# Kernel optimization log

Hardware: AMD Instinct MI355X
Metric: run time of the kernel (lower is better)

## Reference

```python
import jax, jax.numpy as jnp
import numpy as np

B, T, D, E, H = 4, 1024, 1024, 8, 2048


def setup_inputs() -> dict:
    key = jax.random.key(0)
    ks = jax.random.split(key, 5)
    # Kaiming-uniform-ish init scales (exact values irrelevant for correctness baseline)
    bound_bank = 1.0 / np.sqrt(D)
    bound_down = 1.0 / np.sqrt(H)
    return {
        "x": jax.random.normal(ks[0], (B, T, D), dtype=jnp.float32),
        "gate_w": jax.random.uniform(ks[1], (E, D), jnp.float32, -bound_bank, bound_bank),
        "gate_bank": jax.random.uniform(ks[2], (E, D, H), jnp.float32, -bound_bank, bound_bank),
        "up_bank": jax.random.uniform(ks[3], (E, D, H), jnp.float32, -bound_bank, bound_bank),
        "down_bank": jax.random.uniform(ks[4], (E, H, D), jnp.float32, -bound_down, bound_down),
    }


def reference(x, gate_w, gate_bank, up_bank, down_bank):
    # Router logits: [B,T,E] (nn.Linear with weight [E,D], no bias)
    logits = jnp.einsum('btd,ed->bte', x, gate_w)
    selected = jnp.argmax(logits, axis=-1)          # [B,T] int
    # Dense all-expert SwiGLU
    u = jnp.einsum('btd,edh->bteh', x, up_bank)     # [B,T,E,H]
    a = jnp.einsum('btd,edh->bteh', x, gate_bank)   # [B,T,E,H]
    h = jax.nn.silu(a) * u                          # [B,T,E,H]
    y = jnp.einsum('bteh,ehd->bted', h, down_bank)  # [B,T,E,D]
    # Gather argmax-selected expert output per token
    idx = selected[:, :, None, None]                # [B,T,1,1]
    out = jnp.take_along_axis(y, idx, axis=2)[:, :, 0, :]  # [B,T,D]
    return out
```

## Files before the change

kernel.cpp:

```cpp
#include <hip/hip_runtime.h>
#include <hip/hip_bf16.h>

#define NTOK 4096
#define DDIM 1024
#define HDIM 2048
#define NEXP 8

typedef __attribute__((ext_vector_type(4))) float f32x4;
typedef __attribute__((ext_vector_type(8))) short bf16x8;
typedef __attribute__((ext_vector_type(8))) unsigned short us8;

__device__ __forceinline__ unsigned short f2bf(float f) {
    unsigned u = __float_as_uint(f);
    return (unsigned short)((u + 0x7fffu + ((u >> 16) & 1u)) >> 16);
}

__device__ __forceinline__ void gload16(const void* g, void* l) {
    __builtin_amdgcn_global_load_lds((const __attribute__((address_space(1))) void*)g,
                                     (__attribute__((address_space(3))) void*)l, 16, 0, 0);
}

__global__ __launch_bounds__(256) void xg_kernel(
        const float* __restrict__ x, const float* __restrict__ gw,
        unsigned short* __restrict__ xb, int* __restrict__ sel) {
    const int t = blockIdx.x, tid = threadIdx.x, lane = tid & 63, w = tid >> 6;
    const float4 v = *reinterpret_cast<const float4*>(x + (size_t)t * DDIM + tid * 4);
    ushort4 o = { f2bf(v.x), f2bf(v.y), f2bf(v.z), f2bf(v.w) };
    *reinterpret_cast<ushort4*>(xb + (size_t)t * DDIM + tid * 4) = o;

    double acc[NEXP];
    #pragma unroll
    for (int e = 0; e < NEXP; ++e) {
        const float4 g = *reinterpret_cast<const float4*>(gw + (size_t)e * DDIM + tid * 4);
        acc[e] = (double)v.x * g.x + (double)v.y * g.y + (double)v.z * g.z + (double)v.w * g.w;
    }
    __shared__ double red[4][NEXP];
    #pragma unroll
    for (int e = 0; e < NEXP; ++e) {
        double a = acc[e];
        #pragma unroll
        for (int off = 32; off; off >>= 1) a += __shfl_down(a, off);
        if (lane == 0) red[w][e] = a;
    }
    __syncthreads();
    if (tid == 0) {
        int best = 0; double bv = -1e300;
        #pragma unroll
        for (int e = 0; e < NEXP; ++e) {
            double s = red[0][e] + red[1][e] + red[2][e] + red[3][e];
            if (s > bv) { bv = s; best = e; }
        }
        sel[t] = best;
    }
}

__global__ void scatter_kernel(const int* __restrict__ sel, int* __restrict__ cnt,
                               int* __restrict__ perm) {
    int t = blockIdx.x * blockDim.x + threadIdx.x;
    if (t < NTOK) {
        int e = sel[t];
        int p = atomicAdd(&cnt[e], 1);
        perm[e * NTOK + p] = t;
    }
}

__global__ __launch_bounds__(256) void fcast(const float* __restrict__ src,
        unsigned short* __restrict__ dst, int R, int C, int NB, int KS,
        int interleave, int qsel, long long estride) {
    __shared__ unsigned short tile[64][72];
    const int e = blockIdx.z, r0 = blockIdx.y * 64, c0 = blockIdx.x * 64;
    const float* s = src + ((size_t)e * R + r0) * C + c0;
    const int t = threadIdx.x;
    const int rd = t >> 2;
    #pragma unroll
    for (int j = 0; j < 4; ++j) {
        int c4 = (t & 3) * 4 + j;
        float4 v = *reinterpret_cast<const float4*>(s + (size_t)rd * C + c4 * 4);
        tile[c4 * 4 + 0][rd] = f2bf(v.x);
        tile[c4 * 4 + 1][rd] = f2bf(v.y);
        tile[c4 * 4 + 2][rd] = f2bf(v.z);
        tile[c4 * 4 + 3][rd] = f2bf(v.w);
    }
    __syncthreads();
    const int q = t >> 6, l = t & 63, li = l & 15, lg = l >> 4;
    const int nblk = interleave ? (((c0 >> 4) + q) * 2 + qsel) : ((c0 >> 4) + q);
    #pragma unroll
    for (int kf2 = 0; kf2 < 2; ++kf2) {
        const int ks = (r0 >> 5) + kf2;
        us8 v = *reinterpret_cast<const us8*>(&tile[q * 16 + li][kf2 * 32 + lg * 8]);
        *reinterpret_cast<us8*>(dst + ((size_t)e * estride) +
            (((size_t)nblk * KS + ks) << 9) + l * 8) = v;
    }
}

__global__ __launch_bounds__(256, 3) void stage_a(
        const unsigned short* __restrict__ xb, const unsigned short* __restrict__ wa,
        const int* __restrict__ cnt, const int* __restrict__ perm,
        unsigned short* __restrict__ hws) {
    const int e = blockIdx.z;
    const int bx = blockIdx.x;
    const int m0 = blockIdx.y * 128;
    const int count = cnt[e];
    if (m0 >= count) return;
    const int* pl = perm + e * NTOK;

    __shared__ unsigned short __attribute__((aligned(16))) As[2][128 * 64];

    const int tid = threadIdx.x, lane = tid & 63, w = tid >> 6;
    const int wr = w >> 1, wc = w & 1, li = lane & 15, lg = lane >> 4;
    const int sb = lane & 7, r8 = lane >> 3;
    const int srcswz = (sb ^ r8) * 8;

    const unsigned short* pA[4];
    #pragma unroll
    for (int i = 0; i < 4; ++i) {
        int row = i * 32 + w * 8 + r8;
        int tr = m0 + row; if (tr >= count) tr = count - 1;
        pA[i] = xb + (size_t)pl[tr] * DDIM + srcswz;
    }
    const unsigned short* bp = wa + (((size_t)e * 256 + bx * 8 + wc * 4) << 5 << 9)
                               + (size_t)lane * 8;

    f32x4 acc[4][4];
    #pragma unroll
    for (int i = 0; i < 4; ++i)
        #pragma unroll
        for (int j = 0; j < 4; ++j) acc[i][j] = (f32x4){0.f, 0.f, 0.f, 0.f};

    #pragma unroll
    for (int i = 0; i < 4; ++i) gload16(pA[i], &As[0][(i * 256 + w * 64) * 8]);
    asm volatile("s_waitcnt vmcnt(0)" ::: "memory");
    __syncthreads();

    int cur = 0;
    const int NT = DDIM / 64;
    for (int t = 0; t < NT; ++t) {
        if (t + 1 < NT) {
            const int k0 = (t + 1) * 64;
            #pragma unroll
            for (int i = 0; i < 4; ++i) gload16(pA[i] + k0, &As[cur ^ 1][(i * 256 + w * 64) * 8]);
        }
        #pragma unroll
        for (int kf = 0; kf < 2; ++kf) {
            const int kb = kf * 4 + lg;
            bf16x8 a[4], b[4];
            #pragma unroll
            for (int ni = 0; ni < 4; ++ni)
                b[ni] = *reinterpret_cast<const bf16x8*>(bp + (((size_t)(ni * 32 + t * 2 + kf)) << 9));
            #pragma unroll
            for (int mi = 0; mi < 4; ++mi) {
                int r = wr * 64 + mi * 16 + li;
                a[mi] = *reinterpret_cast<const bf16x8*>(&As[cur][r * 64 + ((kb ^ (li & 7)) << 3)]);
            }
            #pragma unroll
            for (int mi = 0; mi < 4; ++mi)
                #pragma unroll
                for (int ni = 0; ni < 4; ++ni)
                    acc[mi][ni] = __builtin_amdgcn_mfma_f32_16x16x32_bf16(a[mi], b[ni], acc[mi][ni], 0, 0, 0);
        }
        if (t + 1 < NT) {
            asm volatile("s_waitcnt vmcnt(0)" ::: "memory");
            __syncthreads();
            cur ^= 1;
        }
    }
    const int hbase = bx * 64 + wc * 32 + li;
    #pragma unroll
    for (int mi = 0; mi < 4; ++mi) {
        #pragma unroll
        for (int r = 0; r < 4; ++r) {
            int row = m0 + wr * 64 + mi * 16 + lg * 4 + r;
            if (row < count) {
                int tok = pl[row];
                #pragma unroll
                for (int p = 0; p < 2; ++p) {
                    float a = acc[mi][p * 2 + 0][r];
                    float u = acc[mi][p * 2 + 1][r];
                    float h = (a / (1.f + __expf(-a))) * u;
                    hws[(size_t)tok * HDIM + hbase + p * 16] = f2bf(h);
                }
            }
        }
    }
}

__global__ __launch_bounds__(256, 3) void stage_b(
        const unsigned short* __restrict__ hws, const unsigned short* __restrict__ wb,
        const int* __restrict__ cnt, const int* __restrict__ perm,
        float* __restrict__ out) {
    const int e = blockIdx.z;
    const int bx = blockIdx.x;
    const int m0 = blockIdx.y * 128;
    const int count = cnt[e];
    if (m0 >= count) return;
    const int* pl = perm + e * NTOK;

    __shared__ unsigned short __attribute__((aligned(16))) As[2][128 * 64];

    const int tid = threadIdx.x, lane = tid & 63, w = tid >> 6;
    const int wr = w >> 1, wc = w & 1, li = lane & 15, lg = lane >> 4;
    const int sb = lane & 7, r8 = lane >> 3;
    const int srcswz = (sb ^ r8) * 8;

    const unsigned short* pA[4];
    #pragma unroll
    for (int i = 0; i < 4; ++i) {
        int row = i * 32 + w * 8 + r8;
        int tr = m0 + row; if (tr >= count) tr = count - 1;
        pA[i] = hws + (size_t)pl[tr] * HDIM + srcswz;
    }
    const unsigned short* bp = wb + (((size_t)e * 64 + bx * 8 + wc * 4) * 64 << 9)
                               + (size_t)lane * 8;

    f32x4 acc[4][4];
    #pragma unroll
    for (int i = 0; i < 4; ++i)
        #pragma unroll
        for (int j = 0; j < 4; ++j) acc[i][j] = (f32x4){0.f, 0.f, 0.f, 0.f};

    #pragma unroll
    for (int i = 0; i < 4; ++i) gload16(pA[i], &As[0][(i * 256 + w * 64) * 8]);
    asm volatile("s_waitcnt vmcnt(0)" ::: "memory");
    __syncthreads();

    int cur = 0;
    const int NT = HDIM / 64;
    for (int t = 0; t < NT; ++t) {
        if (t + 1 < NT) {
            const int k0 = (t + 1) * 64;
            #pragma unroll
            for (int i = 0; i < 4; ++i) gload16(pA[i] + k0, &As[cur ^ 1][(i * 256 + w * 64) * 8]);
        }
        #pragma unroll
        for (int kf = 0; kf < 2; ++kf) {
            const int kb = kf * 4 + lg;
            bf16x8 a[4], b[4];
            #pragma unroll
            for (int ni = 0; ni < 4; ++ni)
                b[ni] = *reinterpret_cast<const bf16x8*>(bp + (((size_t)(ni * 64 + t * 2 + kf)) << 9));
            #pragma unroll
            for (int mi = 0; mi < 4; ++mi) {
                int r = wr * 64 + mi * 16 + li;
                a[mi] = *reinterpret_cast<const bf16x8*>(&As[cur][r * 64 + ((kb ^ (li & 7)) << 3)]);
            }
            #pragma unroll
            for (int mi = 0; mi < 4; ++mi)
                #pragma unroll
                for (int ni = 0; ni < 4; ++ni)
                    acc[mi][ni] = __builtin_amdgcn_mfma_f32_16x16x32_bf16(a[mi], b[ni], acc[mi][ni], 0, 0, 0);
        }
        if (t + 1 < NT) {
            asm volatile("s_waitcnt vmcnt(0)" ::: "memory");
            __syncthreads();
            cur ^= 1;
        }
    }
    const int cbase = bx * 128 + wc * 64 + li;
    #pragma unroll
    for (int mi = 0; mi < 4; ++mi) {
        #pragma unroll
        for (int r = 0; r < 4; ++r) {
            int row = m0 + wr * 64 + mi * 16 + lg * 4 + r;
            if (row < count) {
                int tok = pl[row];
                #pragma unroll
                for (int ni = 0; ni < 4; ++ni)
                    out[(size_t)tok * DDIM + cbase + ni * 16] = acc[mi][ni][r];
            }
        }
    }
}

extern "C" void kernel_launch(void* const* d_in, const int* in_sizes, int n_in,
                              void* d_out, int out_size, void* d_ws, size_t ws_size,
                              hipStream_t stream) {
    const float* x  = (const float*)d_in[0];
    const float* gw = (const float*)d_in[1];
    const float* gb = (const float*)d_in[2];
    const float* ub = (const float*)d_in[3];
    const float* db = (const float*)d_in[4];
    float* out = (float*)d_out;

    char* ws = (char*)d_ws;
    unsigned short* wbank = (unsigned short*)(ws);
    unsigned short* hws   = (unsigned short*)(ws + 67108864);
    unsigned short* xbf   = (unsigned short*)(ws + 67108864 + 16777216);
    char* misc = ws + 67108864 + 16777216 + 8388608;
    int* cnt  = (int*)(misc);
    int* sel  = (int*)(misc + 256);
    int* perm = (int*)(misc + 256 + 16384);

    hipMemsetAsync(cnt, 0, 256, stream);
    xg_kernel<<<NTOK, 256, 0, stream>>>(x, gw, xbf, sel);
    fcast<<<dim3(HDIM / 64, DDIM / 64, NEXP), 256, 0, stream>>>(
        gb, wbank, DDIM, HDIM, 256, 32, 1, 0, (long long)256 * 32 * 512);
    fcast<<<dim3(HDIM / 64, DDIM / 64, NEXP), 256, 0, stream>>>(
        ub, wbank, DDIM, HDIM, 256, 32, 1, 1, (long long)256 * 32 * 512);
    scatter_kernel<<<NTOK / 256, 256, 0, stream>>>(sel, cnt, perm);
    stage_a<<<dim3(2 * HDIM / 128, NTOK / 128, NEXP), 256, 0, stream>>>(
        xbf, wbank, cnt, perm, hws);
    fcast<<<dim3(DDIM / 64, HDIM / 64, NEXP), 256, 0, stream>>>(
        db, wbank, HDIM, DDIM, 64, 64, 0, 0, (long long)64 * 64 * 512);
    stage_b<<<dim3(DDIM / 128, NTOK / 128, NEXP), 256, 0, stream>>>(
        hws, wbank, cnt, perm, out);
}
```

Before: 382.4 us.

## Split-K down projection with atomics, smaller tiles, and LDS-free weight cast

The down-projection kernel now uses 64-row tiles and splits the H reduction into two halves across grid z, so it launches more blocks to fill the device. Partial sums are combined with float atomicAdd into an output that is zeroed beforehand. The weight cast kernel drops its LDS transpose and reads strided columns directly into the packed bf16 layout, and both GEMM stages request occupancy 4. In exchange, the output is written twice through atomics and needs an extra memset, results become order-nondeterministic, and the cast's column reads are less coalesced.

```diff
diff --git a/kernel.cpp b/kernel.cpp
--- a/kernel.cpp
+++ b/kernel.cpp
@@ -65,35 +65,22 @@
 }
 
 __global__ __launch_bounds__(256) void fcast(const float* __restrict__ src,
-        unsigned short* __restrict__ dst, int R, int C, int NB, int KS,
+        unsigned short* __restrict__ dst, int C, int KS, int NB,
         int interleave, int qsel, long long estride) {
-    __shared__ unsigned short tile[64][72];
-    const int e = blockIdx.z, r0 = blockIdx.y * 64, c0 = blockIdx.x * 64;
-    const float* s = src + ((size_t)e * R + r0) * C + c0;
-    const int t = threadIdx.x;
-    const int rd = t >> 2;
-    #pragma unroll
-    for (int j = 0; j < 4; ++j) {
-        int c4 = (t & 3) * 4 + j;
-        float4 v = *reinterpret_cast<const float4*>(s + (size_t)rd * C + c4 * 4);
-        tile[c4 * 4 + 0][rd] = f2bf(v.x);
-        tile[c4 * 4 + 1][rd] = f2bf(v.y);
-        tile[c4 * 4 + 2][rd] = f2bf(v.z);
-        tile[c4 * 4 + 3][rd] = f2bf(v.w);
-    }
-    __syncthreads();
-    const int q = t >> 6, l = t & 63, li = l & 15, lg = l >> 4;
-    const int nblk = interleave ? (((c0 >> 4) + q) * 2 + qsel) : ((c0 >> 4) + q);
-    #pragma unroll
-    for (int kf2 = 0; kf2 < 2; ++kf2) {
-        const int ks = (r0 >> 5) + kf2;
-        us8 v = *reinterpret_cast<const us8*>(&tile[q * 16 + li][kf2 * 32 + lg * 8]);
-        *reinterpret_cast<us8*>(dst + ((size_t)e * estride) +
-            (((size_t)nblk * KS + ks) << 9) + l * 8) = v;
-    }
-}
-
-__global__ __launch_bounds__(256, 3) void stage_a(
+    const int e = blockIdx.z, cblk = blockIdx.x;
+    const int w = threadIdx.x >> 6, l = threadIdx.x & 63;
+    const int ks = blockIdx.y * 4 + w;
+    const int li = l & 15, lg = l >> 4;
+    const int nblk = interleave ? cblk * 2 + qsel : cblk;
+    const float* s = src + ((size_t)e * KS * 32 + ks * 32 + lg * 8) * C + cblk * 16 + li;
+    unsigned short v[8];
+    #pragma unroll
+    for (int j = 0; j < 8; ++j) v[j] = f2bf(s[(size_t)j * C]);
+    *reinterpret_cast<us8*>(dst + (size_t)e * estride +
+        (((size_t)nblk * KS + ks) << 9) + l * 8) = *reinterpret_cast<const us8*>(v);
+}
+
+__global__ __launch_bounds__(256, 4) void stage_a(
         const unsigned short* __restrict__ xb, const unsigned short* __restrict__ wa,
         const int* __restrict__ cnt, const int* __restrict__ perm,
         unsigned short* __restrict__ hws) {
@@ -184,69 +171,69 @@
     }
 }
 
-__global__ __launch_bounds__(256, 3) void stage_b(
+__global__ __launch_bounds__(256, 4) void stage_b(
         const unsigned short* __restrict__ hws, const unsigned short* __restrict__ wb,
         const int* __restrict__ cnt, const int* __restrict__ perm,
         float* __restrict__ out) {
-    const int e = blockIdx.z;
+    const int z = blockIdx.z, e = z >> 1, kz = z & 1;
     const int bx = blockIdx.x;
-    const int m0 = blockIdx.y * 128;
+    const int m0 = blockIdx.y * 64;
     const int count = cnt[e];
     if (m0 >= count) return;
     const int* pl = perm + e * NTOK;
 
-    __shared__ unsigned short __attribute__((aligned(16))) As[2][128 * 64];
-
-    const int tid = threadIdx.x, lane = tid & 63, w = tid >> 6;
-    const int wr = w >> 1, wc = w & 1, li = lane & 15, lg = lane >> 4;
+    __shared__ unsigned short __attribute__((aligned(16))) As[2][64 * 64];
+
+    const int tid = threadIdx.x, lane = tid & 63, wc = tid >> 6;
+    const int li = lane & 15, lg = lane >> 4;
     const int sb = lane & 7, r8 = lane >> 3;
     const int srcswz = (sb ^ r8) * 8;
 
-    const unsigned short* pA[4];
-    #pragma unroll
-    for (int i = 0; i < 4; ++i) {
-        int row = i * 32 + w * 8 + r8;
+    const unsigned short* pA[2];
+    #pragma unroll
+    for (int i = 0; i < 2; ++i) {
+        int row = wc * 16 + i * 8 + r8;
         int tr = m0 + row; if (tr >= count) tr = count - 1;
-        pA[i] = hws + (size_t)pl[tr] * HDIM + srcswz;
-    }
-    const unsigned short* bp = wb + (((size_t)e * 64 + bx * 8 + wc * 4) * 64 << 9)
-                               + (size_t)lane * 8;
-
-    f32x4 acc[4][4];
+        pA[i] = hws + (size_t)pl[tr] * HDIM + kz * 1024 + srcswz;
+    }
+    const unsigned short* bp = wb + ((((size_t)e * 64 + bx * 8 + wc * 2) * 64
+                               + (size_t)kz * 32) << 9) + (size_t)lane * 8;
+
+    f32x4 acc[4][2];
     #pragma unroll
     for (int i = 0; i < 4; ++i)
         #pragma unroll
-        for (int j = 0; j < 4; ++j) acc[i][j] = (f32x4){0.f, 0.f, 0.f, 0.f};
-
-    #pragma unroll
-    for (int i = 0; i < 4; ++i) gload16(pA[i], &As[0][(i * 256 + w * 64) * 8]);
+        for (int j = 0; j < 2; ++j) acc[i][j] = (f32x4){0.f, 0.f, 0.f, 0.f};
+
+    #pragma unroll
+    for (int i = 0; i < 2; ++i) gload16(pA[i], &As[0][(wc * 2 + i) * 512]);
     asm volatile("s_waitcnt vmcnt(0)" ::: "memory");
     __syncthreads();
 
     int cur = 0;
-    const int NT = HDIM / 64;
+    const int NT = 16;
     for (int t = 0; t < NT; ++t) {
         if (t + 1 < NT) {
             const int k0 = (t + 1) * 64;
             #pragma unroll
-            for (int i = 0; i < 4; ++i) gload16(pA[i] + k0, &As[cur ^ 1][(i * 256 + w * 64) * 8]);
+            for (int i = 0; i < 2; ++i) gload16(pA[i] + k0, &As[cur ^ 1][(wc * 2 + i) * 512]);
         }
         #pragma unroll
         for (int kf = 0; kf < 2; ++kf) {
             const int kb = kf * 4 + lg;
-            bf16x8 a[4], b[4];
-            #pragma unroll
-            for (int ni = 0; ni < 4; ++ni)
+            bf16x8 a[4], b[2];
+            #pragma unroll
+            for (int ni = 0; ni < 2; ++ni)
                 b[ni] = *reinterpret_cast<const bf16x8*>(bp + (((size_t)(ni * 64 + t * 2 + kf)) << 9));
             #pragma unroll
             for (int mi = 0; mi < 4; ++mi) {
-                int r = wr * 64 + mi * 16 + li;
+                int r = mi * 16 + li;
                 a[mi] = *reinterpret_cast<const bf16x8*>(&As[cur][r * 64 + ((kb ^ (li & 7)) << 3)]);
             }
             #pragma unroll
             for (int mi = 0; mi < 4; ++mi)
                 #pragma unroll
-                for (int ni = 0; ni < 4; ++ni)
+                for (int ni = 0; ni < 2; ++ni)
                     acc[mi][ni] = __builtin_amdgcn_mfma_f32_16x16x32_bf16(a[mi], b[ni], acc[mi][ni], 0, 0, 0);
         }
         if (t + 1 < NT) {
@@ -255,17 +242,17 @@
             cur ^= 1;
         }
     }
-    const int cbase = bx * 128 + wc * 64 + li;
+    const int cbase = bx * 128 + wc * 32 + li;
     #pragma unroll
     for (int mi = 0; mi < 4; ++mi) {
         #pragma unroll
         for (int r = 0; r < 4; ++r) {
-            int row = m0 + wr * 64 + mi * 16 + lg * 4 + r;
+            int row = m0 + mi * 16 + lg * 4 + r;
             if (row < count) {
                 int tok = pl[row];
                 #pragma unroll
-                for (int ni = 0; ni < 4; ++ni)
-                    out[(size_t)tok * DDIM + cbase + ni * 16] = acc[mi][ni][r];
+                for (int ni = 0; ni < 2; ++ni)
+                    atomicAdd(&out[(size_t)tok * DDIM + cbase + ni * 16], acc[mi][ni][r]);
             }
         }
     }
@@ -292,15 +279,16 @@
 
     hipMemsetAsync(cnt, 0, 256, stream);
     xg_kernel<<<NTOK, 256, 0, stream>>>(x, gw, xbf, sel);
-    fcast<<<dim3(HDIM / 64, DDIM / 64, NEXP), 256, 0, stream>>>(
-        gb, wbank, DDIM, HDIM, 256, 32, 1, 0, (long long)256 * 32 * 512);
-    fcast<<<dim3(HDIM / 64, DDIM / 64, NEXP), 256, 0, stream>>>(
-        ub, wbank, DDIM, HDIM, 256, 32, 1, 1, (long long)256 * 32 * 512);
+    fcast<<<dim3(HDIM / 16, 32 / 4, NEXP), 256, 0, stream>>>(
+        gb, wbank, HDIM, 32, 256, 1, 0, (long long)256 * 32 * 512);
+    fcast<<<dim3(HDIM / 16, 32 / 4, NEXP), 256, 0, stream>>>(
+        ub, wbank, HDIM, 32, 256, 1, 1, (long long)256 * 32 * 512);
     scatter_kernel<<<NTOK / 256, 256, 0, stream>>>(sel, cnt, perm);
     stage_a<<<dim3(2 * HDIM / 128, NTOK / 128, NEXP), 256, 0, stream>>>(
         xbf, wbank, cnt, perm, hws);
-    fcast<<<dim3(DDIM / 64, HDIM / 64, NEXP), 256, 0, stream>>>(
-        db, wbank, HDIM, DDIM, 64, 64, 0, 0, (long long)64 * 64 * 512);
-    stage_b<<<dim3(DDIM / 128, NTOK / 128, NEXP), 256, 0, stream>>>(
+    fcast<<<dim3(DDIM / 16, 64 / 4, NEXP), 256, 0, stream>>>(
+        db, wbank, DDIM, 64, 64, 0, 0, (long long)64 * 64 * 512);
+    hipMemsetAsync(out, 0, (size_t)NTOK * DDIM * 4, stream);
+    stage_b<<<dim3(DDIM / 128, NTOK / 64, NEXP * 2), 256, 0, stream>>>(
         hws, wbank, cnt, perm, out);
 }
```

Result: no change. 388.8 us (+1.7%).
